# Performance work log

Measured on AMD Instinct MI355X. Metric: run time of the kernel, lower is better.

Reference implementation:

```python
import jax, jax.numpy as jnp
import numpy as np

D_K = 256.0  # K_dim from __init__, used only as 1/sqrt(d_k) scale


def setup_inputs() -> dict:
    key = jax.random.key(0)
    ks = jax.random.split(key, 8)
    B, S, L, DQ, DK, DV, H = 8, 4096, 64, 1024, 1024, 1024, 256
    Q = jax.random.normal(ks[0], (B, S, DQ), dtype=jnp.float32)
    K = jax.random.normal(ks[1], (L, DK), dtype=jnp.float32)
    V = jax.random.normal(ks[2], (B, S, DV), dtype=jnp.float32)
    attn_mask = jax.random.randint(ks[3], (B, S, 1), 0, 2).astype(jnp.bool_)
    Wq_w = jax.random.normal(ks[4], (H, DQ), dtype=jnp.float32) * 0.02
    Wq_b = jnp.zeros((H,), dtype=jnp.float32)
    Wk_w = jax.random.normal(ks[5], (H, DK), dtype=jnp.float32) * 0.02
    Wk_b = jnp.zeros((H,), dtype=jnp.float32)
    return {"Q": Q, "K": K, "V": V, "attn_mask": attn_mask,
            "Wq_w": Wq_w, "Wq_b": Wq_b, "Wk_w": Wk_w, "Wk_b": Wk_b}


def reference(Q, K, V, attn_mask, Wq_w, Wq_b, Wk_w, Wk_b):
    # Projections (the original's expand/repeat + mul + sum is exactly a GEMM)
    kh = K @ Wk_w.T + Wk_b                                  # (L, 256)
    qh = (Q @ Wq_w.T + Wq_b) / jnp.sqrt(jnp.float32(D_K))   # (B, S, 256)
    # S[b,s,l] = sum_d qh[b,s,d]*kh[l,d]; scores sums over labels too
    S = jnp.einsum('bsd,ld->bsl', qh, kh)                   # (B, S, L)
    scores = S.sum(-1)[..., None] + attn_mask.astype(jnp.float32) * (-1e9)  # (B,S,1)
    scores = jnp.swapaxes(scores, -1, -2)                   # (B, 1, S)
    attn = jax.nn.softmax(scores, axis=-1)                  # (B, 1, S)
    context = jnp.matmul(attn, V)[:, 0, :]                  # (B, DV)
    return context, attn
```

## Files before the change

### kernel.cpp

```cpp
#include <hip/hip_runtime.h>
#include <hip/hip_bf16.h>
#include <cstddef>


#define B 8
#define S 4096
#define DQ 1024
#define H 256
#define L 64
#define RPB 16
#define SC2 16
#define NSC2 (S / SC2)


__global__ void ksumc_kernel(const float* __restrict__ K, float* __restrict__ ks_c) {
    int c = blockIdx.x * 64 + threadIdx.x;
    float acc = 0.f;
#pragma unroll 8
    for (int l = 0; l < L; ++l) acc += K[l * DQ + c];
    ks_c[c] = acc;
}

__global__ void ksum_kernel(const float* __restrict__ Wk_w, const float* __restrict__ Wk_b,
                            const float* __restrict__ ks_c, float* __restrict__ ksum) {
    __shared__ float sv[DQ];
    for (int i = threadIdx.x; i < DQ; i += 256) sv[i] = ks_c[i];
    __syncthreads();
    int wave = threadIdx.x >> 6, lane = threadIdx.x & 63;
    int d = blockIdx.x * 4 + wave;
    const float* wr = Wk_w + (size_t)d * DQ;
    float acc = 0.f;
#pragma unroll
    for (int j = 0; j < 4; ++j) {
        int idx = j * 256 + lane * 4;
        float4 a = *(const float4*)(wr + idx);
        float4 b = *(const float4*)(sv + idx);
        acc += a.x * b.x + a.y * b.y + a.z * b.z + a.w * b.w;
    }
    for (int off = 32; off; off >>= 1) acc += __shfl_down(acc, off);
    if (lane == 0) ksum[d] = acc + 64.f * Wk_b[d];
}

__global__ void wvec_bias_kernel(const float* __restrict__ Wq_w, const float* __restrict__ Wq_b,
                                 const float* __restrict__ ksum, float* __restrict__ w,
                                 float* __restrict__ bias) {
    __shared__ float ks[H];
    __shared__ float red[4][64];
    __shared__ float red2[4];
    ks[threadIdx.x] = ksum[threadIdx.x];
    __syncthreads();
    int wave = threadIdx.x >> 6, lane = threadIdx.x & 63;
    if (blockIdx.x < 16) {
        int c = blockIdx.x * 64 + lane;
        float acc = 0.f;
#pragma unroll 8
        for (int j = 0; j < 64; ++j) {
            int d = wave + 4 * j;
            acc += Wq_w[(size_t)d * DQ + c] * ks[d];
        }
        red[wave][lane] = acc;
        __syncthreads();
        if (wave == 0)
            w[c] = (red[0][lane] + red[1][lane] + red[2][lane] + red[3][lane]) * 0.0625f;
    } else {
        float v = Wq_b[threadIdx.x] * ks[threadIdx.x];
        for (int off = 32; off; off >>= 1) v += __shfl_down(v, off);
        if (lane == 0) red2[wave] = v;
        __syncthreads();
        if (threadIdx.x == 0)
            bias[0] = (red2[0] + red2[1] + red2[2] + red2[3]) * 0.0625f;
    }
}

__global__ __launch_bounds__(256) void scores_kernel(
        const float* __restrict__ Q, const float* __restrict__ w,
        const float* __restrict__ bias, const int* __restrict__ mask,
        float* __restrict__ escore, float* __restrict__ denom) {
    int t = threadIdx.x;
    size_t base = (size_t)blockIdx.x * RPB;
    float4 wv = *(const float4*)(w + t * 4);
    __shared__ float sp[RPB * 256];
    __shared__ float bsum[RPB];
    const float* qb = Q + base * DQ + t * 4;

    float4 qv[RPB];
#pragma unroll
    for (int r = 0; r < RPB; ++r) qv[r] = *(const float4*)(qb + (size_t)r * DQ);
#pragma unroll
    for (int r = 0; r < RPB; ++r)
        sp[r * 256 + t] = qv[r].x * wv.x + qv[r].y * wv.y + qv[r].z * wv.z + qv[r].w * wv.w;
    __syncthreads();

    int r = t >> 4, j = t & 15;
    float s = 0.f;
#pragma unroll
    for (int k = 0; k < 16; ++k) s += sp[r * 256 + k * 16 + j];
    s += __shfl_xor(s, 8, 64);
    s += __shfl_xor(s, 4, 64);
    s += __shfl_xor(s, 2, 64);
    s += __shfl_xor(s, 1, 64);
    if (j == 0) {
        size_t row = base + r;
        float e = mask[row] ? 0.f : __expf(s + bias[0]);
        escore[row] = e;
        bsum[r] = e;
    }
    __syncthreads();
    if (t == 0) {
        float d0 = 0.f;
#pragma unroll
        for (int k = 0; k < RPB; ++k) d0 += bsum[k];
        atomicAdd(denom + (base >> 12), d0);
    }
}

__global__ __launch_bounds__(256) void ctx_partial_kernel(
        const float* __restrict__ V, const float* __restrict__ escore,
        float* __restrict__ partial) {
    int sc = blockIdx.x, b = blockIdx.y, t = threadIdx.x;
    __shared__ float es[SC2];
    if (t < SC2) es[t] = escore[(size_t)b * S + sc * SC2 + t];
    __syncthreads();
    const float* vb = V + ((size_t)b * S + (size_t)sc * SC2) * DQ + t * 4;
    float4 acc = {0.f, 0.f, 0.f, 0.f};
#pragma unroll
    for (int s0 = 0; s0 < SC2; s0 += 8) {
        float4 v[8];
#pragma unroll
        for (int k = 0; k < 8; ++k) v[k] = *(const float4*)(vb + (size_t)(s0 + k) * DQ);
#pragma unroll
        for (int k = 0; k < 8; ++k) {
            float a = es[s0 + k];
            acc.x += a * v[k].x; acc.y += a * v[k].y;
            acc.z += a * v[k].z; acc.w += a * v[k].w;
        }
    }
    *(float4*)(partial + ((size_t)b * NSC2 + sc) * DQ + t * 4) = acc;
}

__global__ void epilogue_kernel(const float* __restrict__ escore, const float* __restrict__ partial,
                                const float* __restrict__ denom,
                                float* __restrict__ ctx, float* __restrict__ attn) {
    if (blockIdx.x < 128) {
        int i = blockIdx.x * 256 + threadIdx.x;
        attn[i] = escore[i] / denom[i >> 12];
    } else {
        int idx = (blockIdx.x - 128) * 256 + threadIdx.x;
        int b = idx >> 10, d = idx & 1023;
        const float* p = partial + (size_t)b * NSC2 * DQ + d;
        float acc = 0.f;
#pragma unroll 8
        for (int sc = 0; sc < NSC2; ++sc) acc += p[(size_t)sc * DQ];
        ctx[idx] = acc / denom[b];
    }
}

extern "C" void kernel_launch(void* const* d_in, const int* in_sizes, int n_in,
                              void* d_out, int out_size, void* d_ws, size_t ws_size,
                              hipStream_t stream) {
    const float* Q    = (const float*)d_in[0];
    const float* K    = (const float*)d_in[1];
    const float* V    = (const float*)d_in[2];
    const int*   mask = (const int*)d_in[3];
    const float* Wq_w = (const float*)d_in[4];
    const float* Wq_b = (const float*)d_in[5];
    const float* Wk_w = (const float*)d_in[6];
    const float* Wk_b = (const float*)d_in[7];

    float* ws     = (float*)d_ws;
    float* ks_c   = ws;
    float* ksum   = ws + 1024;
    float* wv     = ws + 1280;
    float* bias   = ws + 2304;
    float* denom  = ws + 2312;
    float* escore = ws + 4096;
    float* partial = ws + 4096 + B * S;

    float* ctx  = (float*)d_out;
    float* attn = (float*)d_out + B * DQ;

    hipMemsetAsync(denom, 0, B * sizeof(float), stream);
    ksumc_kernel<<<16, 64, 0, stream>>>(K, ks_c);
    ksum_kernel<<<H / 4, 256, 0, stream>>>(Wk_w, Wk_b, ks_c, ksum);
    wvec_bias_kernel<<<17, 256, 0, stream>>>(Wq_w, Wq_b, ksum, wv, bias);
    scores_kernel<<<(B * S) / RPB, 256, 0, stream>>>(Q, wv, bias, mask, escore, denom);
    ctx_partial_kernel<<<dim3(NSC2, B), 256, 0, stream>>>(V, escore, partial);
    epilogue_kernel<<<160, 256, 0, stream>>>(escore, partial, denom, ctx, attn);
}
```

Measured before the change: 323.1 us.

## Fuse score and context-partial kernels; merge K column-sum into ksum kernel

The scores kernel and the context-partial kernel are merged into one kernel. Each block computes exp-scores for its 16 rows and then immediately accumulates those rows of V, so the escore re-read and one launch go away. The K column-sum is folded into the ksum kernel, with each of 64 blocks recomputing it redundantly, and the denom memset moves into that kernel. The cost is one fewer pipeline stage of overlap and more work per block in the main kernel.

```diff
diff --git a/kernel.cpp b/kernel.cpp
--- a/kernel.cpp
+++ b/kernel.cpp
@@ -9,41 +9,43 @@
 #define H 256
 #define L 64
 #define RPB 16
-#define SC2 16
-#define NSC2 (S / SC2)
+#define NSC (S / RPB)
 
-
-__global__ void ksumc_kernel(const float* __restrict__ K, float* __restrict__ ks_c) {
-    int c = blockIdx.x * 64 + threadIdx.x;
-    float acc = 0.f;
+__global__ __launch_bounds__(256) void pre1_kernel(
+        const float* __restrict__ K, const float* __restrict__ Wk_w,
+        const float* __restrict__ Wk_b, float* __restrict__ ksum,
+        float* __restrict__ denom) {
+    __shared__ float sv[DQ];
+    int t = threadIdx.x;
+    if (blockIdx.x == 0 && t < B) denom[t] = 0.f;
+    float4 a = {0.f, 0.f, 0.f, 0.f};
+    const float* kp = K + t * 4;
 #pragma unroll 8
-    for (int l = 0; l < L; ++l) acc += K[l * DQ + c];
-    ks_c[c] = acc;
-}
-
-__global__ void ksum_kernel(const float* __restrict__ Wk_w, const float* __restrict__ Wk_b,
-                            const float* __restrict__ ks_c, float* __restrict__ ksum) {
-    __shared__ float sv[DQ];
-    for (int i = threadIdx.x; i < DQ; i += 256) sv[i] = ks_c[i];
+    for (int l = 0; l < L; ++l) {
+        float4 k = *(const float4*)(kp + (size_t)l * DQ);
+        a.x += k.x; a.y += k.y; a.z += k.z; a.w += k.w;
+    }
+    *(float4*)(sv + t * 4) = a;
     __syncthreads();
-    int wave = threadIdx.x >> 6, lane = threadIdx.x & 63;
+    int wave = t >> 6, lane = t & 63;
     int d = blockIdx.x * 4 + wave;
     const float* wr = Wk_w + (size_t)d * DQ;
     float acc = 0.f;
 #pragma unroll
     for (int j = 0; j < 4; ++j) {
         int idx = j * 256 + lane * 4;
-        float4 a = *(const float4*)(wr + idx);
-        float4 b = *(const float4*)(sv + idx);
-        acc += a.x * b.x + a.y * b.y + a.z * b.z + a.w * b.w;
+        float4 x = *(const float4*)(wr + idx);
+        float4 y = *(const float4*)(sv + idx);
+        acc += x.x * y.x + x.y * y.y + x.z * y.z + x.w * y.w;
     }
     for (int off = 32; off; off >>= 1) acc += __shfl_down(acc, off);
     if (lane == 0) ksum[d] = acc + 64.f * Wk_b[d];
 }
 
-__global__ void wvec_bias_kernel(const float* __restrict__ Wq_w, const float* __restrict__ Wq_b,
-                                 const float* __restrict__ ksum, float* __restrict__ w,
-                                 float* __restrict__ bias) {
+__global__ __launch_bounds__(256) void pre2_kernel(
+        const float* __restrict__ Wq_w, const float* __restrict__ Wq_b,
+        const float* __restrict__ ksum, float* __restrict__ w,
+        float* __restrict__ bias) {
     __shared__ float ks[H];
     __shared__ float red[4][64];
     __shared__ float red2[4];
@@ -72,17 +74,19 @@
     }
 }
 
-__global__ __launch_bounds__(256) void scores_kernel(
-        const float* __restrict__ Q, const float* __restrict__ w,
-        const float* __restrict__ bias, const int* __restrict__ mask,
-        float* __restrict__ escore, float* __restrict__ denom) {
-    int t = threadIdx.x;
-    size_t base = (size_t)blockIdx.x * RPB;
+__global__ __launch_bounds__(256) void fused_main_kernel(
+        const float* __restrict__ Q, const float* __restrict__ V,
+        const float* __restrict__ w, const float* __restrict__ bias,
+        const int* __restrict__ mask,
+        float* __restrict__ escore, float* __restrict__ denom,
+        float* __restrict__ partial) {
+    int sc = blockIdx.x, b = blockIdx.y, t = threadIdx.x;
+    __shared__ float sp[RPB * 256];
+    __shared__ float es[RPB];
+    size_t rowbase = (size_t)b * S + (size_t)sc * RPB;
+
+    const float* qb = Q + rowbase * DQ + t * 4;
     float4 wv = *(const float4*)(w + t * 4);
-    __shared__ float sp[RPB * 256];
-    __shared__ float bsum[RPB];
-    const float* qb = Q + base * DQ + t * 4;
-
     float4 qv[RPB];
 #pragma unroll
     for (int r = 0; r < RPB; ++r) qv[r] = *(const float4*)(qb + (size_t)r * DQ);
@@ -100,31 +104,23 @@
     s += __shfl_xor(s, 2, 64);
     s += __shfl_xor(s, 1, 64);
     if (j == 0) {
-        size_t row = base + r;
+        size_t row = rowbase + r;
         float e = mask[row] ? 0.f : __expf(s + bias[0]);
+        es[r] = e;
         escore[row] = e;
-        bsum[r] = e;
     }
     __syncthreads();
     if (t == 0) {
         float d0 = 0.f;
 #pragma unroll
-        for (int k = 0; k < RPB; ++k) d0 += bsum[k];
-        atomicAdd(denom + (base >> 12), d0);
+        for (int k = 0; k < RPB; ++k) d0 += es[k];
+        atomicAdd(denom + b, d0);
     }
-}
 
-__global__ __launch_bounds__(256) void ctx_partial_kernel(
-        const float* __restrict__ V, const float* __restrict__ escore,
-        float* __restrict__ partial) {
-    int sc = blockIdx.x, b = blockIdx.y, t = threadIdx.x;
-    __shared__ float es[SC2];
-    if (t < SC2) es[t] = escore[(size_t)b * S + sc * SC2 + t];
-    __syncthreads();
-    const float* vb = V + ((size_t)b * S + (size_t)sc * SC2) * DQ + t * 4;
+    const float* vb = V + rowbase * DQ + t * 4;
     float4 acc = {0.f, 0.f, 0.f, 0.f};
 #pragma unroll
-    for (int s0 = 0; s0 < SC2; s0 += 8) {
+    for (int s0 = 0; s0 < RPB; s0 += 8) {
         float4 v[8];
 #pragma unroll
         for (int k = 0; k < 8; ++k) v[k] = *(const float4*)(vb + (size_t)(s0 + k) * DQ);
@@ -135,22 +131,23 @@
             acc.z += a * v[k].z; acc.w += a * v[k].w;
         }
     }
-    *(float4*)(partial + ((size_t)b * NSC2 + sc) * DQ + t * 4) = acc;
+    *(float4*)(partial + ((size_t)b * NSC + sc) * DQ + t * 4) = acc;
 }
 
-__global__ void epilogue_kernel(const float* __restrict__ escore, const float* __restrict__ partial,
-                                const float* __restrict__ denom,
-                                float* __restrict__ ctx, float* __restrict__ attn) {
+__global__ __launch_bounds__(256) void epilogue_kernel(
+        const float* __restrict__ escore, const float* __restrict__ partial,
+        const float* __restrict__ denom,
+        float* __restrict__ ctx, float* __restrict__ attn) {
     if (blockIdx.x < 128) {
         int i = blockIdx.x * 256 + threadIdx.x;
         attn[i] = escore[i] / denom[i >> 12];
     } else {
         int idx = (blockIdx.x - 128) * 256 + threadIdx.x;
         int b = idx >> 10, d = idx & 1023;
-        const float* p = partial + (size_t)b * NSC2 * DQ + d;
+        const float* p = partial + (size_t)b * NSC * DQ + d;
         float acc = 0.f;
 #pragma unroll 8
-        for (int sc = 0; sc < NSC2; ++sc) acc += p[(size_t)sc * DQ];
+        for (int sc = 0; sc < NSC; ++sc) acc += p[(size_t)sc * DQ];
         ctx[idx] = acc / denom[b];
     }
 }
@@ -168,22 +165,19 @@
     const float* Wk_b = (const float*)d_in[7];
 
     float* ws     = (float*)d_ws;
-    float* ks_c   = ws;
-    float* ksum   = ws + 1024;
-    float* wv     = ws + 1280;
-    float* bias   = ws + 2304;
-    float* denom  = ws + 2312;
+    float* ksum   = ws;
+    float* wv     = ws + 256;
+    float* bias   = ws + 1280;
+    float* denom  = ws + 1288;
     float* escore = ws + 4096;
     float* partial = ws + 4096 + B * S;
 
     float* ctx  = (float*)d_out;
     float* attn = (float*)d_out + B * DQ;
 
-    hipMemsetAsync(denom, 0, B * sizeof(float), stream);
-    ksumc_kernel<<<16, 64, 0, stream>>>(K, ks_c);
-    ksum_kernel<<<H / 4, 256, 0, stream>>>(Wk_w, Wk_b, ks_c, ksum);
-    wvec_bias_kernel<<<17, 256, 0, stream>>>(Wq_w, Wq_b, ksum, wv, bias);
-    scores_kernel<<<(B * S) / RPB, 256, 0, stream>>>(Q, wv, bias, mask, escore, denom);
-    ctx_partial_kernel<<<dim3(NSC2, B), 256, 0, stream>>>(V, escore, partial);
+    pre1_kernel<<<H / 4, 256, 0, stream>>>(K, Wk_w, Wk_b, ksum, denom);
+    pre2_kernel<<<17, 256, 0, stream>>>(Wq_w, Wq_b, ksum, wv, bias);
+    fused_main_kernel<<<dim3(NSC, B), 256, 0, stream>>>(Q, V, wv, bias, mask,
+                                                        escore, denom, partial);
     epilogue_kernel<<<160, 256, 0, stream>>>(escore, partial, denom, ctx, attn);
 }
```

Result: no change. 319.3 us (-1.2%).
